# Performance work log

Hardware: AMD Instinct MI355X
Metric: run time of the kernel (lower is better)

## Reference

```python
import jax, jax.numpy as jnp
import numpy as np

N_NODES = 50000
N_EDGES = 300000
IN_CH = 128
HIDDEN = 64
OUT_CH = 40
NUM_LAYERS = 4
HEADS = 8


def setup_inputs() -> dict:
    key = jax.random.key(0)
    ks = jax.random.split(key, 8)
    s = lambda fan_in: 1.0 / np.sqrt(fan_in)
    return {
        "x": jax.random.normal(ks[0], (N_NODES, IN_CH), dtype=jnp.float32),
        "edge_index": jax.random.randint(ks[1], (2, N_EDGES), 0, N_NODES, dtype=jnp.int64),
        "heads": HEADS,
        "w1": jax.random.uniform(ks[2], (IN_CH, HIDDEN), jnp.float32, -s(IN_CH), s(IN_CH)),
        "b1": jnp.zeros((HIDDEN,), jnp.float32),
        "wq": jax.random.uniform(ks[3], (NUM_LAYERS, HIDDEN, HIDDEN), jnp.float32, -s(HIDDEN), s(HIDDEN)),
        "wk": jax.random.uniform(ks[4], (NUM_LAYERS, HIDDEN, HIDDEN), jnp.float32, -s(HIDDEN), s(HIDDEN)),
        "wv": jax.random.uniform(ks[5], (NUM_LAYERS, HIDDEN, HIDDEN), jnp.float32, -s(HIDDEN), s(HIDDEN)),
        "w2": jax.random.uniform(ks[6], (HIDDEN, OUT_CH), jnp.float32, -s(HIDDEN), s(HIDDEN)),
        "b2": jnp.zeros((OUT_CH,), jnp.float32),
    }


def _dna_conv(x_all, src, dst, norm, wq, wk, wv, heads):
    # x_all: [N, L, C]; attention of each node's latest state over neighbors' full history.
    N, L, C = x_all.shape
    d = C // heads
    q = (x_all[:, -1] @ wq).reshape(N, heads, d)      # [N, h, d]
    k = (x_all @ wk).reshape(N, L, heads, d)          # [N, L, h, d]
    v = (x_all @ wv).reshape(N, L, heads, d)
    qe = q[dst]                                       # [E, h, d]
    ke = k[src]                                       # [E, L, h, d]
    ve = v[src]
    scale = 1.0 / jnp.sqrt(jnp.asarray(d, x_all.dtype))
    score = jnp.einsum('ehd,elhd->ehl', qe, ke) * scale
    attn = jax.nn.softmax(score, axis=-1)             # softmax over history L
    msg = jnp.einsum('ehl,elhd->ehd', attn, ve).reshape(-1, C)
    msg = msg * norm[:, None]                         # GCN symmetric norm per edge
    return jax.ops.segment_sum(msg, dst, num_segments=N)  # sum-aggregate at target


def reference(x, edge_index, heads, w1, b1, wq, wk, wv, w2, b2):
    N = x.shape[0]
    loop = jnp.arange(N, dtype=edge_index.dtype)
    src = jnp.concatenate([edge_index[0], loop])      # gcn_norm adds self loops
    dst = jnp.concatenate([edge_index[1], loop])
    ew = jnp.ones(src.shape[0], x.dtype)
    deg = jax.ops.segment_sum(ew, dst, num_segments=N)
    dinv = jnp.where(deg > 0, jax.lax.rsqrt(deg), 0.0)
    norm = dinv[src] * dinv[dst]

    h = jax.nn.relu(x @ w1 + b1)                      # lin1 + ReLU (DFALayer = identity fwd)
    x_all = h[:, None, :]                             # [N, 1, C]
    for i in range(wq.shape[0]):
        out = jax.nn.relu(_dna_conv(x_all, src, dst, norm, wq[i], wk[i], wv[i], heads))
        x_all = jnp.concatenate([x_all, out[:, None, :]], axis=1)
    logits = x_all[:, -1] @ w2 + b2
    return jax.nn.log_softmax(logits, axis=1)
```

## Files before the change

### kernel.cpp

```cpp
#include <hip/hip_runtime.h>
#include <hip/hip_fp16.h>
#include <math.h>

#define N_NODES 50000
#define N_EDGES 300000
#define E_TOT (N_EDGES + N_NODES)
#define IN_CH 128
#define HIDDEN 64
#define OUT_CH 40
#define NUM_LAYERS 4
#define NCHUNK ((N_NODES + 255) / 256)
#define NTILES (N_NODES / 16)
#define QKV_WPR 512

typedef _Float16 h8 __attribute__((ext_vector_type(8)));
typedef float f32x4 __attribute__((ext_vector_type(4)));
typedef float f32x2 __attribute__((ext_vector_type(2)));

#define MFMA16(a, b, c) __builtin_amdgcn_mfma_f32_16x16x32_f16((a), (b), (c), 0, 0, 0)

__global__ void k_count_init(int* count, int* fill) {
    int n = blockIdx.x * blockDim.x + threadIdx.x;
    if (n < N_NODES) { count[n] = 1; fill[n] = 1; }
}

__global__ void k_count(const int* __restrict__ dst, int* count) {
    int e = blockIdx.x * blockDim.x + threadIdx.x;
    if (e < N_EDGES) atomicAdd(&count[dst[e]], 1);
}

__global__ __launch_bounds__(256) void k_scan_a(const int* __restrict__ count,
                                                int* __restrict__ loc,
                                                int* __restrict__ psum) {
    __shared__ int s[256];
    int tid = threadIdx.x;
    int g = blockIdx.x * 256 + tid;
    int v = (g < N_NODES) ? count[g] : 0;
    s[tid] = v;
    __syncthreads();
    for (int off = 1; off < 256; off <<= 1) {
        int t = (tid >= off) ? s[tid - off] : 0;
        __syncthreads();
        s[tid] += t;
        __syncthreads();
    }
    if (g < N_NODES) loc[g] = s[tid] - v;
    if (tid == 255) psum[blockIdx.x] = s[255];
}

__global__ __launch_bounds__(256) void k_scan_b(int* psum) {
    __shared__ int s[256];
    int tid = threadIdx.x;
    int v = (tid < NCHUNK) ? psum[tid] : 0;
    s[tid] = v;
    __syncthreads();
    for (int off = 1; off < 256; off <<= 1) {
        int t = (tid >= off) ? s[tid - off] : 0;
        __syncthreads();
        s[tid] += t;
        __syncthreads();
    }
    if (tid < NCHUNK) psum[tid] = s[tid] - v;
}

__global__ void k_scan_c(const int* __restrict__ count, const int* __restrict__ loc,
                         const int* __restrict__ psum, int* __restrict__ rowptr,
                         float* __restrict__ dinv, int2* __restrict__ edata) {
    int n = blockIdx.x * blockDim.x + threadIdx.x;
    if (n >= N_NODES) return;
    int rp = loc[n] + psum[n >> 8];
    rowptr[n] = rp;
    float di = rsqrtf((float)count[n]);
    dinv[n] = di;
    edata[rp] = make_int2(n, __float_as_int(di * di));
    if (n == 0) rowptr[N_NODES] = E_TOT;
}

__global__ void k_scatter(const int* __restrict__ ei, const int* __restrict__ rowptr,
                          int* __restrict__ fill, const float* __restrict__ dinv,
                          int2* __restrict__ edata) {
    int e = blockIdx.x * blockDim.x + threadIdx.x;
    if (e >= N_EDGES) return;
    int s = ei[e], d = ei[N_EDGES + e];
    int p = rowptr[d] + atomicAdd(&fill[d], 1);
    edata[p] = make_int2(s, __float_as_int(dinv[s] * dinv[d]));
}

__device__ __forceinline__ h8 load_bfrag(const float* __restrict__ W, int ncols,
                                         int kbase, int c) {
    h8 r;
#pragma unroll
    for (int i = 0; i < 8; ++i) r[i] = (_Float16)W[(kbase + i) * ncols + c];
    return r;
}

__device__ __forceinline__ void unpack8(float4 raw, float* f) {
    const __half2* hp = (const __half2*)&raw;
#pragma unroll
    for (int i = 0; i < 4; ++i) {
        float2 t = __half22float2(hp[i]);
        f[2 * i] = t.x;
        f[2 * i + 1] = t.y;
    }
}

__device__ __forceinline__ void unpack8_fp8(uint2 raw, float* f) {
    f32x2 t;
    t = __builtin_amdgcn_cvt_pk_f32_fp8(raw.x, false); f[0] = t[0]; f[1] = t[1];
    t = __builtin_amdgcn_cvt_pk_f32_fp8(raw.x, true);  f[2] = t[0]; f[3] = t[1];
    t = __builtin_amdgcn_cvt_pk_f32_fp8(raw.y, false); f[4] = t[0]; f[5] = t[1];
    t = __builtin_amdgcn_cvt_pk_f32_fp8(raw.y, true);  f[6] = t[0]; f[7] = t[1];
}

__device__ __forceinline__ int pack4_fp8(float a, float b, float c, float d) {
    int r = __builtin_amdgcn_cvt_pk_fp8_f32(a, b, 0, false);
    r = __builtin_amdgcn_cvt_pk_fp8_f32(c, d, r, true);
    return r;
}

__device__ __forceinline__ float2 pack4(float a, float b, float c, float d) {
    union { __half2 h2[2]; float2 f2; } u;
    u.h2[0] = __floats2half2_rn(a, b);
    u.h2[1] = __floats2half2_rn(c, d);
    return u.f2;
}

__global__ __launch_bounds__(256) void k_h_mfma(const float* __restrict__ x,
                                                const float* __restrict__ w1,
                                                const float* __restrict__ b1,
                                                __half* __restrict__ xh) {
    int lane = threadIdx.x & 63;
    int gw = blockIdx.x * 4 + (threadIdx.x >> 6);
    int krow = lane >> 4, col = lane & 15;
    h8 B[4][4];
#pragma unroll
    for (int ct = 0; ct < 4; ++ct)
#pragma unroll
        for (int s = 0; s < 4; ++s)
            B[ct][s] = load_bfrag(w1, HIDDEN, krow * 8 + 32 * s, ct * 16 + col);
    float4 bias[4];
#pragma unroll
    for (int ct = 0; ct < 4; ++ct) bias[ct] = *(const float4*)&b1[ct * 16 + krow * 4];
    for (int t = gw; t < NTILES; t += 1024) {
        int n0 = t * 16;
        const float* xrow = x + (size_t)(n0 + col) * IN_CH + krow * 8;
        f32x4 acc[4] = {{0.f, 0.f, 0.f, 0.f}, {0.f, 0.f, 0.f, 0.f},
                        {0.f, 0.f, 0.f, 0.f}, {0.f, 0.f, 0.f, 0.f}};
#pragma unroll
        for (int s = 0; s < 4; ++s) {
            float4 p0 = *(const float4*)(xrow + 32 * s);
            float4 p1 = *(const float4*)(xrow + 32 * s + 4);
            h8 a;
            a[0] = (_Float16)p0.x; a[1] = (_Float16)p0.y;
            a[2] = (_Float16)p0.z; a[3] = (_Float16)p0.w;
            a[4] = (_Float16)p1.x; a[5] = (_Float16)p1.y;
            a[6] = (_Float16)p1.z; a[7] = (_Float16)p1.w;
#pragma unroll
            for (int ct = 0; ct < 4; ++ct) acc[ct] = MFMA16(B[ct][s], a, acc[ct]);
        }
        __half* op = xh + (size_t)(n0 + col) * 320 + krow * 4;
#pragma unroll
        for (int ct = 0; ct < 4; ++ct) {
            float2 pk = pack4(fmaxf(acc[ct][0] + bias[ct].x, 0.f),
                              fmaxf(acc[ct][1] + bias[ct].y, 0.f),
                              fmaxf(acc[ct][2] + bias[ct].z, 0.f),
                              fmaxf(acc[ct][3] + bias[ct].w, 0.f));
            *(float2*)(op + ct * 16) = pk;
        }
    }
}

__global__ __launch_bounds__(256) void k_v1_mfma(const __half* __restrict__ xh,
                                                 const float* __restrict__ wv,
                                                 __half* __restrict__ vh1) {
    int lane = threadIdx.x & 63;
    int gw = blockIdx.x * 4 + (threadIdx.x >> 6);
    int krow = lane >> 4, col = lane & 15;
    h8 B[4][2];
#pragma unroll
    for (int ct = 0; ct < 4; ++ct)
#pragma unroll
        for (int s = 0; s < 2; ++s)
            B[ct][s] = load_bfrag(wv, HIDDEN, krow * 8 + 32 * s, ct * 16 + col);
    for (int t = gw; t < NTILES; t += QKV_WPR) {
        int n0 = t * 16;
        const __half* ap = xh + (size_t)(n0 + col) * 320 + krow * 8;
        h8 a0 = *(const h8*)(const void*)ap;
        h8 a1 = *(const h8*)(const void*)(ap + 32);
        f32x4 acc[4] = {{0.f, 0.f, 0.f, 0.f}, {0.f, 0.f, 0.f, 0.f},
                        {0.f, 0.f, 0.f, 0.f}, {0.f, 0.f, 0.f, 0.f}};
#pragma unroll
        for (int ct = 0; ct < 4; ++ct) {
            acc[ct] = MFMA16(B[ct][0], a0, acc[ct]);
            acc[ct] = MFMA16(B[ct][1], a1, acc[ct]);
        }
        __half* op = vh1 + (size_t)(n0 + col) * 64 + krow * 4;
#pragma unroll
        for (int ct = 0; ct < 4; ++ct)
            *(float2*)(op + ct * 16) =
                pack4(acc[ct][0], acc[ct][1], acc[ct][2], acc[ct][3]);
    }
}

__global__ __launch_bounds__(256) void k_edge_l1(const int* __restrict__ rowptr,
                                                 const int2* __restrict__ edata,
                                                 const __half* __restrict__ vh1,
                                                 __half* __restrict__ xh) {
    int tid = threadIdx.x;
    int wid = tid >> 6, lane = tid & 63;
    int g = lane >> 3, r = lane & 7;
    int d = blockIdx.x * 4 + wid;
    if (d >= N_NODES) return;
    int rs = rowptr[d], re = rowptr[d + 1];
    float acc[8];
#pragma unroll
    for (int i = 0; i < 8; ++i) acc[i] = 0.f;
    for (int base = rs; base < re; base += 8) {
        int eidx = base + g;
        bool valid = eidx < re;
        int2 e = edata[valid ? eidx : rs];
        int s = e.x;
        float nrm = valid ? __int_as_float(e.y) : 0.f;
        float4 raw = *(const float4*)(vh1 + (size_t)s * 64 + r * 8);
        float f[8];
        unpack8(raw, f);
#pragma unroll
        for (int c = 0; c < 8; ++c) acc[c] = fmaf(nrm, f[c], acc[c]);
    }
#pragma unroll
    for (int c = 0; c < 8; ++c) {
        acc[c] += __shfl_xor(acc[c], 8);
        acc[c] += __shfl_xor(acc[c], 16);
        acc[c] += __shfl_xor(acc[c], 32);
    }
    if (lane < 8) {
        __half hbuf[8];
#pragma unroll
        for (int c = 0; c < 8; ++c) hbuf[c] = __float2half(fmaxf(acc[c], 0.f));
        *(float4*)(xh + (size_t)d * 320 + 64 + r * 8) = *(float4*)hbuf;
    }
}

template <int L>
__global__ __launch_bounds__(256) void k_qkv_mfma(const __half* __restrict__ xh,
                                                  const float* __restrict__ wq,
                                                  const float* __restrict__ wk,
                                                  const float* __restrict__ wv,
                                                  __half* __restrict__ qh,
                                                  unsigned char* __restrict__ kvi) {
    int lane = threadIdx.x & 63;
    int gw = blockIdx.x * 4 + (threadIdx.x >> 6);
    int lx = gw / QKV_WPR;
    int slot = gw - lx * QKV_WPR;
    int krow = lane >> 4, col = lane & 15;
    bool doq = (lx == L - 1);
    h8 Bk[4][2], Bv[4][2], Bq[4][2];
#pragma unroll
    for (int ct = 0; ct < 4; ++ct)
#pragma unroll
        for (int s = 0; s < 2; ++s) {
            Bk[ct][s] = load_bfrag(wk, HIDDEN, krow * 8 + 32 * s, ct * 16 + col);
            Bv[ct][s] = load_bfrag(wv, HIDDEN, krow * 8 + 32 * s, ct * 16 + col);
        }
    if (doq) {
#pragma unroll
        for (int ct = 0; ct < 4; ++ct)
#pragma unroll
            for (int s = 0; s < 2; ++s)
                Bq[ct][s] = load_bfrag(wq, HIDDEN, krow * 8 + 32 * s, ct * 16 + col);
    }
    for (int t = slot; t < NTILES; t += QKV_WPR) {
        int n0 = t * 16;
        const __half* ap = xh + (size_t)(n0 + col) * 320 + lx * 64 + krow * 8;
        h8 a0 = *(const h8*)(const void*)ap;
        h8 a1 = *(const h8*)(const void*)(ap + 32);
        f32x4 ak[4] = {{0.f, 0.f, 0.f, 0.f}, {0.f, 0.f, 0.f, 0.f},
                       {0.f, 0.f, 0.f, 0.f}, {0.f, 0.f, 0.f, 0.f}};
        f32x4 av[4] = {{0.f, 0.f, 0.f, 0.f}, {0.f, 0.f, 0.f, 0.f},
                       {0.f, 0.f, 0.f, 0.f}, {0.f, 0.f, 0.f, 0.f}};
#pragma unroll
        for (int ct = 0; ct < 4; ++ct) {
            ak[ct] = MFMA16(Bk[ct][0], a0, ak[ct]);
            ak[ct] = MFMA16(Bk[ct][1], a1, ak[ct]);
            av[ct] = MFMA16(Bv[ct][0], a0, av[ct]);
            av[ct] = MFMA16(Bv[ct][1], a1, av[ct]);
        }
        unsigned char* op = kvi + ((size_t)(n0 + col) * L + lx) * 128 + krow * 4;
#pragma unroll
        for (int ct = 0; ct < 4; ++ct) {
            *(int*)(op + ct * 16) = pack4_fp8(ak[ct][0], ak[ct][1], ak[ct][2], ak[ct][3]);
            *(int*)(op + 64 + ct * 16) = pack4_fp8(av[ct][0], av[ct][1], av[ct][2], av[ct][3]);
        }
        if (doq) {
            f32x4 aq[4] = {{0.f, 0.f, 0.f, 0.f}, {0.f, 0.f, 0.f, 0.f},
                           {0.f, 0.f, 0.f, 0.f}, {0.f, 0.f, 0.f, 0.f}};
#pragma unroll
            for (int ct = 0; ct < 4; ++ct) {
                aq[ct] = MFMA16(Bq[ct][0], a0, aq[ct]);
                aq[ct] = MFMA16(Bq[ct][1], a1, aq[ct]);
            }
            const float scl = 0.35355339059327373f;
            __half* qp = qh + (size_t)(n0 + col) * 64 + krow * 4;
#pragma unroll
            for (int ct = 0; ct < 4; ++ct)
                *(float2*)(qp + ct * 16) = pack4(aq[ct][0] * scl, aq[ct][1] * scl,
                                                 aq[ct][2] * scl, aq[ct][3] * scl);
        }
    }
}

template <int L>
__global__ __launch_bounds__(256) void k_edge_csr8(const int* __restrict__ rowptr,
                                                   const int2* __restrict__ edata,
                                                   const unsigned char* __restrict__ kvi,
                                                   const __half* __restrict__ qh,
                                                   float* __restrict__ aggout,
                                                   __half* __restrict__ xh) {
    int tid = threadIdx.x;
    int wid = tid >> 6, lane = tid & 63;
    int g = lane >> 3, r = lane & 7;
    int d = blockIdx.x * 4 + wid;
    if (d >= N_NODES) return;
    int rs = rowptr[d], re = rowptr[d + 1];
    float qf[8];
    unpack8(((const float4*)(qh + (size_t)d * 64))[r], qf);
    float acc[8];
#pragma unroll
    for (int i = 0; i < 8; ++i) acc[i] = 0.f;
    for (int base = rs; base < re; base += 8) {
        int eidx = base + g;
        bool valid = eidx < re;
        int2 e = edata[valid ? eidx : rs];
        int s = e.x;
        float nrm = valid ? __int_as_float(e.y) : 0.f;
        float sc[L];
        uint2 vraw[L];
        const unsigned char* kb = kvi + (size_t)s * (L * 128) + r * 8;
#pragma unroll
        for (int l = 0; l < L; ++l) {
            uint2 kraw = *(const uint2*)(kb + l * 128);
            vraw[l] = *(const uint2*)(kb + l * 128 + 64);
            float kf[8];
            unpack8_fp8(kraw, kf);
            float p = 0.f;
#pragma unroll
            for (int c = 0; c < 8; ++c) p = fmaf(qf[c], kf[c], p);
            sc[l] = p;
        }
        float m = sc[0];
#pragma unroll
        for (int l = 1; l < L; ++l) m = fmaxf(m, sc[l]);
        float ssum = 0.f;
#pragma unroll
        for (int l = 0; l < L; ++l) { sc[l] = __expf(sc[l] - m); ssum += sc[l]; }
        float w = __fdividef(nrm, ssum);
#pragma unroll
        for (int l = 0; l < L; ++l) {
            float swl = sc[l] * w;
            float vf[8];
            unpack8_fp8(vraw[l], vf);
#pragma unroll
            for (int c = 0; c < 8; ++c) acc[c] = fmaf(swl, vf[c], acc[c]);
        }
    }
#pragma unroll
    for (int c = 0; c < 8; ++c) {
        acc[c] += __shfl_xor(acc[c], 8);
        acc[c] += __shfl_xor(acc[c], 16);
        acc[c] += __shfl_xor(acc[c], 32);
    }
    if (lane < 8) {
        if (L == NUM_LAYERS) {
            float4 o0, o1;
            o0.x = fmaxf(acc[0], 0.f); o0.y = fmaxf(acc[1], 0.f);
            o0.z = fmaxf(acc[2], 0.f); o0.w = fmaxf(acc[3], 0.f);
            o1.x = fmaxf(acc[4], 0.f); o1.y = fmaxf(acc[5], 0.f);
            o1.z = fmaxf(acc[6], 0.f); o1.w = fmaxf(acc[7], 0.f);
            float4* op = (float4*)(aggout + (size_t)d * 64 + r * 8);
            op[0] = o0; op[1] = o1;
        } else {
            __half hbuf[8];
#pragma unroll
            for (int c = 0; c < 8; ++c) hbuf[c] = __float2half(fmaxf(acc[c], 0.f));
            *(float4*)(xh + (size_t)d * 320 + L * 64 + r * 8) = *(float4*)hbuf;
        }
    }
}

__global__ __launch_bounds__(256) void k_final_lds(const float* __restrict__ aggout,
                                                   const float* __restrict__ w2,
                                                   const float* __restrict__ b2,
                                                   float* __restrict__ out) {
    __shared__ float rows[16][HIDDEN];
    int tid = threadIdx.x, wid = tid >> 6, lane = tid & 63;
    int cl = (lane < OUT_CH) ? lane : (OUT_CH - 1);
    float wcol[HIDDEN];
#pragma unroll
    for (int j = 0; j < HIDDEN; ++j) wcol[j] = w2[j * OUT_CH + cl];
    float b = b2[cl];
    for (int t = blockIdx.x; t < NTILES; t += gridDim.x) {
        int n0 = t * 16;
        {
            int rr = tid >> 4, seg = tid & 15;
            *(float4*)&rows[rr][seg * 4] =
                *(const float4*)&aggout[(size_t)(n0 + rr) * 64 + seg * 4];
        }
        __syncthreads();
#pragma unroll
        for (int u = 0; u < 4; ++u) {
            int ln = wid * 4 + u;
            const float4* rp = (const float4*)rows[ln];
            float a0 = 0.f, a1 = 0.f, a2 = 0.f, a3 = 0.f;
#pragma unroll
            for (int jc = 0; jc < HIDDEN / 4; ++jc) {
                float4 r = rp[jc];
                a0 = fmaf(r.x, wcol[jc * 4 + 0], a0);
                a1 = fmaf(r.y, wcol[jc * 4 + 1], a1);
                a2 = fmaf(r.z, wcol[jc * 4 + 2], a2);
                a3 = fmaf(r.w, wcol[jc * 4 + 3], a3);
            }
            float logit = (lane < OUT_CH) ? ((a0 + a1) + (a2 + a3) + b) : -INFINITY;
            float m = logit;
            for (int mask = 32; mask; mask >>= 1) m = fmaxf(m, __shfl_xor(m, mask));
            float ex = (lane < OUT_CH) ? __expf(logit - m) : 0.f;
            float ssum = ex;
            for (int mask = 32; mask; mask >>= 1) ssum += __shfl_xor(ssum, mask);
            if (lane < OUT_CH)
                out[(size_t)(n0 + ln) * OUT_CH + lane] = logit - m - logf(ssum);
        }
        __syncthreads();
    }
}

extern "C" void kernel_launch(void* const* d_in, const int* in_sizes, int n_in,
                              void* d_out, int out_size, void* d_ws, size_t ws_size,
                              hipStream_t stream) {
    const float* x  = (const float*)d_in[0];
    const int*   ei = (const int*)d_in[1];
    const float* w1 = (const float*)d_in[3];
    const float* b1 = (const float*)d_in[4];
    const float* wq = (const float*)d_in[5];
    const float* wk = (const float*)d_in[6];
    const float* wv = (const float*)d_in[7];
    const float* w2 = (const float*)d_in[8];
    const float* b2 = (const float*)d_in[9];
    float* out = (float*)d_out;

    char* cur = (char*)d_ws;
    auto alloc = [&](size_t bytes) { char* p = cur; cur += (bytes + 255) & ~(size_t)255; return p; };
    float*         dinv   = (float*)alloc(N_NODES * 4);
    __half*        xh     = (__half*)alloc((size_t)N_NODES * 320 * 2);
    float*         aggout = (float*)alloc((size_t)N_NODES * 64 * 4);
    __half*        qh     = (__half*)alloc((size_t)N_NODES * 64 * 2);
    unsigned char* kvi    = (unsigned char*)alloc((size_t)N_NODES * NUM_LAYERS * 128);
    __half*        vh1    = (__half*)alloc((size_t)N_NODES * 64 * 2);
    int*           count  = (int*)alloc(N_NODES * 4);
    int*           loc    = (int*)alloc(N_NODES * 4);
    int*           psum   = (int*)alloc(256 * 4);
    int*           rowptr = (int*)alloc((N_NODES + 1) * 4);
    int*           fill   = (int*)alloc(N_NODES * 4);
    int2*          edata  = (int2*)alloc((size_t)E_TOT * 8);

    k_count_init<<<(N_NODES + 255) / 256, 256, 0, stream>>>(count, fill);
    k_count<<<(N_EDGES + 255) / 256, 256, 0, stream>>>(ei + N_EDGES, count);
    k_scan_a<<<NCHUNK, 256, 0, stream>>>(count, loc, psum);
    k_scan_b<<<1, 256, 0, stream>>>(psum);
    k_scan_c<<<(N_NODES + 255) / 256, 256, 0, stream>>>(count, loc, psum, rowptr,
                                                        dinv, edata);
    k_scatter<<<(N_EDGES + 255) / 256, 256, 0, stream>>>(ei, rowptr, fill, dinv, edata);

    k_h_mfma<<<256, 256, 0, stream>>>(x, w1, b1, xh);

    k_v1_mfma<<<QKV_WPR / 4, 256, 0, stream>>>(xh, wv, vh1);
    k_edge_l1<<<(N_NODES + 3) / 4, 256, 0, stream>>>(rowptr, edata, vh1, xh);

    for (int i = 1; i < NUM_LAYERS; ++i) {
        int L = i + 1;
        int qkvblk = L * (QKV_WPR / 4);
        const float* wqi = wq + i * 4096;
        const float* wki = wk + i * 4096;
        const float* wvi = wv + i * 4096;
        switch (L) {
            case 2:
                k_qkv_mfma<2><<<qkvblk, 256, 0, stream>>>(xh, wqi, wki, wvi, qh, kvi);
                k_edge_csr8<2><<<(N_NODES + 3) / 4, 256, 0, stream>>>(rowptr, edata, kvi, qh, aggout, xh);
                break;
            case 3:
                k_qkv_mfma<3><<<qkvblk, 256, 0, stream>>>(xh, wqi, wki, wvi, qh, kvi);
                k_edge_csr8<3><<<(N_NODES + 3) / 4, 256, 0, stream>>>(rowptr, edata, kvi, qh, aggout, xh);
                break;
            default:
                k_qkv_mfma<4><<<qkvblk, 256, 0, stream>>>(xh, wqi, wki, wvi, qh, kvi);
                k_edge_csr8<4><<<(N_NODES + 3) / 4, 256, 0, stream>>>(rowptr, edata, kvi, qh, aggout, xh);
                break;
        }
    }
    k_final_lds<<<512, 256, 0, stream>>>(aggout, w2, b2, out);
}
```

Baseline: 254.7 us.

## Store layer-1 V in fp8 and process two edges per iteration in gathers

Layer-1 value vectors are now stored as fp8 instead of fp16, halving the bytes gathered per edge in the first edge kernel. Both edge kernels also process two edge batches per loop iteration, issuing loads for both before computing, to expose more memory-level parallelism. The change adds fp8 quantization error to layer 1 and raises register pressure in the attention kernels.

```diff
diff --git a/kernel.cpp b/kernel.cpp
--- a/kernel.cpp
+++ b/kernel.cpp
@@ -172,7 +172,7 @@
 
 __global__ __launch_bounds__(256) void k_v1_mfma(const __half* __restrict__ xh,
                                                  const float* __restrict__ wv,
-                                                 __half* __restrict__ vh1) {
+                                                 unsigned char* __restrict__ vh1) {
     int lane = threadIdx.x & 63;
     int gw = blockIdx.x * 4 + (threadIdx.x >> 6);
     int krow = lane >> 4, col = lane & 15;
@@ -194,17 +194,17 @@
             acc[ct] = MFMA16(B[ct][0], a0, acc[ct]);
             acc[ct] = MFMA16(B[ct][1], a1, acc[ct]);
         }
-        __half* op = vh1 + (size_t)(n0 + col) * 64 + krow * 4;
+        unsigned char* op = vh1 + (size_t)(n0 + col) * 64 + krow * 4;
 #pragma unroll
         for (int ct = 0; ct < 4; ++ct)
-            *(float2*)(op + ct * 16) =
-                pack4(acc[ct][0], acc[ct][1], acc[ct][2], acc[ct][3]);
+            *(int*)(op + ct * 16) =
+                pack4_fp8(acc[ct][0], acc[ct][1], acc[ct][2], acc[ct][3]);
     }
 }
 
 __global__ __launch_bounds__(256) void k_edge_l1(const int* __restrict__ rowptr,
                                                  const int2* __restrict__ edata,
-                                                 const __half* __restrict__ vh1,
+                                                 const unsigned char* __restrict__ vh1,
                                                  __half* __restrict__ xh) {
     int tid = threadIdx.x;
     int wid = tid >> 6, lane = tid & 63;
@@ -215,17 +215,35 @@
     float acc[8];
 #pragma unroll
     for (int i = 0; i < 8; ++i) acc[i] = 0.f;
-    for (int base = rs; base < re; base += 8) {
-        int eidx = base + g;
-        bool valid = eidx < re;
-        int2 e = edata[valid ? eidx : rs];
-        int s = e.x;
-        float nrm = valid ? __int_as_float(e.y) : 0.f;
-        float4 raw = *(const float4*)(vh1 + (size_t)s * 64 + r * 8);
-        float f[8];
-        unpack8(raw, f);
-#pragma unroll
-        for (int c = 0; c < 8; ++c) acc[c] = fmaf(nrm, f[c], acc[c]);
+    int base = rs;
+    for (; base + 8 < re; base += 16) {
+        int ea = base + g, eb = base + 8 + g;
+        bool va = ea < re, vb = eb < re;
+        int2 e0 = edata[va ? ea : rs];
+        int2 e1 = edata[vb ? eb : rs];
+        float n0 = va ? __int_as_float(e0.y) : 0.f;
+        float n1 = vb ? __int_as_float(e1.y) : 0.f;
+        uint2 raw0 = *(const uint2*)(vh1 + (size_t)e0.x * 64 + r * 8);
+        uint2 raw1 = *(const uint2*)(vh1 + (size_t)e1.x * 64 + r * 8);
+        float f0[8], f1[8];
+        unpack8_fp8(raw0, f0);
+        unpack8_fp8(raw1, f1);
+#pragma unroll
+        for (int c = 0; c < 8; ++c) {
+            acc[c] = fmaf(n0, f0[c], acc[c]);
+            acc[c] = fmaf(n1, f1[c], acc[c]);
+        }
+    }
+    if (base < re) {
+        int ea = base + g;
+        bool va = ea < re;
+        int2 e0 = edata[va ? ea : rs];
+        float n0 = va ? __int_as_float(e0.y) : 0.f;
+        uint2 raw0 = *(const uint2*)(vh1 + (size_t)e0.x * 64 + r * 8);
+        float f0[8];
+        unpack8_fp8(raw0, f0);
+#pragma unroll
+        for (int c = 0; c < 8; ++c) acc[c] = fmaf(n0, f0[c], acc[c]);
     }
 #pragma unroll
     for (int c = 0; c < 8; ++c) {
@@ -306,6 +324,36 @@
                 *(float2*)(qp + ct * 16) = pack4(aq[ct][0] * scl, aq[ct][1] * scl,
                                                  aq[ct][2] * scl, aq[ct][3] * scl);
         }
+    }
+}
+
+template <int L>
+__device__ __forceinline__ void attn_acc(const uint2* kraw, const uint2* vraw,
+                                         float nrm, const float* qf, float* acc) {
+    float sc[L];
+#pragma unroll
+    for (int l = 0; l < L; ++l) {
+        float kf[8];
+        unpack8_fp8(kraw[l], kf);
+        float p = 0.f;
+#pragma unroll
+        for (int c = 0; c < 8; ++c) p = fmaf(qf[c], kf[c], p);
+        sc[l] = p;
+    }
+    float m = sc[0];
+#pragma unroll
+    for (int l = 1; l < L; ++l) m = fmaxf(m, sc[l]);
+    float ssum = 0.f;
+#pragma unroll
+    for (int l = 0; l < L; ++l) { sc[l] = __expf(sc[l] - m); ssum += sc[l]; }
+    float w = __fdividef(nrm, ssum);
+#pragma unroll
+    for (int l = 0; l < L; ++l) {
+        float swl = sc[l] * w;
+        float vf[8];
+        unpack8_fp8(vraw[l], vf);
+#pragma unroll
+        for (int c = 0; c < 8; ++c) acc[c] = fmaf(swl, vf[c], acc[c]);
     }
 }
 
@@ -327,41 +375,40 @@
     float acc[8];
 #pragma unroll
     for (int i = 0; i < 8; ++i) acc[i] = 0.f;
-    for (int base = rs; base < re; base += 8) {
-        int eidx = base + g;
-        bool valid = eidx < re;
-        int2 e = edata[valid ? eidx : rs];
-        int s = e.x;
-        float nrm = valid ? __int_as_float(e.y) : 0.f;
-        float sc[L];
-        uint2 vraw[L];
-        const unsigned char* kb = kvi + (size_t)s * (L * 128) + r * 8;
+    int base = rs;
+    for (; base + 8 < re; base += 16) {
+        int ea = base + g, eb = base + 8 + g;
+        bool va = ea < re, vb = eb < re;
+        int2 e0 = edata[va ? ea : rs];
+        int2 e1 = edata[vb ? eb : rs];
+        float n0 = va ? __int_as_float(e0.y) : 0.f;
+        float n1 = vb ? __int_as_float(e1.y) : 0.f;
+        const unsigned char* kb0 = kvi + (size_t)e0.x * (L * 128) + r * 8;
+        const unsigned char* kb1 = kvi + (size_t)e1.x * (L * 128) + r * 8;
+        uint2 kraw0[L], vraw0[L], kraw1[L], vraw1[L];
 #pragma unroll
         for (int l = 0; l < L; ++l) {
-            uint2 kraw = *(const uint2*)(kb + l * 128);
-            vraw[l] = *(const uint2*)(kb + l * 128 + 64);
-            float kf[8];
-            unpack8_fp8(kraw, kf);
-            float p = 0.f;
-#pragma unroll
-            for (int c = 0; c < 8; ++c) p = fmaf(qf[c], kf[c], p);
-            sc[l] = p;
-        }
-        float m = sc[0];
-#pragma unroll
-        for (int l = 1; l < L; ++l) m = fmaxf(m, sc[l]);
-        float ssum = 0.f;
-#pragma unroll
-        for (int l = 0; l < L; ++l) { sc[l] = __expf(sc[l] - m); ssum += sc[l]; }
-        float w = __fdividef(nrm, ssum);
+            kraw0[l] = *(const uint2*)(kb0 + l * 128);
+            vraw0[l] = *(const uint2*)(kb0 + l * 128 + 64);
+            kraw1[l] = *(const uint2*)(kb1 + l * 128);
+            vraw1[l] = *(const uint2*)(kb1 + l * 128 + 64);
+        }
+        attn_acc<L>(kraw0, vraw0, n0, qf, acc);
+        attn_acc<L>(kraw1, vraw1, n1, qf, acc);
+    }
+    if (base < re) {
+        int ea = base + g;
+        bool va = ea < re;
+        int2 e0 = edata[va ? ea : rs];
+        float n0 = va ? __int_as_float(e0.y) : 0.f;
+        const unsigned char* kb0 = kvi + (size_t)e0.x * (L * 128) + r * 8;
+        uint2 kraw0[L], vraw0[L];
 #pragma unroll
         for (int l = 0; l < L; ++l) {
-            float swl = sc[l] * w;
-            float vf[8];
-            unpack8_fp8(vraw[l], vf);
-#pragma unroll
-            for (int c = 0; c < 8; ++c) acc[c] = fmaf(swl, vf[c], acc[c]);
-        }
+            kraw0[l] = *(const uint2*)(kb0 + l * 128);
+            vraw0[l] = *(const uint2*)(kb0 + l * 128 + 64);
+        }
+        attn_acc<L>(kraw0, vraw0, n0, qf, acc);
     }
 #pragma unroll
     for (int c = 0; c < 8; ++c) {
@@ -453,7 +500,7 @@
     float*         aggout = (float*)alloc((size_t)N_NODES * 64 * 4);
     __half*        qh     = (__half*)alloc((size_t)N_NODES * 64 * 2);
     unsigned char* kvi    = (unsigned char*)alloc((size_t)N_NODES * NUM_LAYERS * 128);
-    __half*        vh1    = (__half*)alloc((size_t)N_NODES * 64 * 2);
+    unsigned char* vh1    = (unsigned char*)alloc((size_t)N_NODES * 64);
     int*           count  = (int*)alloc(N_NODES * 4);
     int*           loc    = (int*)alloc(N_NODES * 4);
     int*           psum   = (int*)alloc(256 * 4);
```

Result: faster. 248.4 us, median of 2 (-2.5%).
